# Optimization experiments

Measured on AMD Instinct MI355X. Metric: run time of the kernel, lower is better.

## Reference

```python
import jax, jax.numpy as jnp
import numpy as np

B, P, ENC = 128, 196, 2048
A, E, D, V, L = 512, 512, 512, 10000, 52


def setup_inputs() -> dict:
    key = jax.random.key(0)
    ks = jax.random.split(key, 20)
    encoder_out = jax.random.normal(ks[0], (B, P, ENC), jnp.float32)
    encoded_captions = jax.random.randint(ks[1], (B, L), 0, V)
    lengths = jax.random.randint(ks[2], (B, 1), 20, L + 1)
    lengths = lengths.at[0, 0].set(L)  # guarantee max(decode_lengths) == L-1
    s = 0.05
    return {
        "encoder_out": encoder_out,
        "encoded_captions": encoded_captions,
        "caption_lengths": lengths,
        "emb": jax.random.uniform(ks[3], (V, E), jnp.float32, -0.1, 0.1),
        "We": jax.random.normal(ks[4], (A, ENC)) * s,   # attention.encoder_att
        "be": jnp.zeros((A,), jnp.float32),
        "Wd": jax.random.normal(ks[5], (A, D)) * s,     # attention.decoder_att
        "bd": jnp.zeros((A,), jnp.float32),
        "wf": jax.random.normal(ks[6], (1, A)) * s,     # attention.full_att
        "bf": jnp.zeros((1,), jnp.float32),
        "W_ih": jax.random.normal(ks[7], (4 * D, E + ENC)) * s,
        "b_ih": jnp.zeros((4 * D,), jnp.float32),
        "W_hh": jax.random.normal(ks[8], (4 * D, D)) * s,
        "b_hh": jnp.zeros((4 * D,), jnp.float32),
        "Wbeta": jax.random.normal(ks[9], (ENC, D)) * s,  # f_beta
        "bbeta": jnp.zeros((ENC,), jnp.float32),
        "Wfc": jax.random.uniform(ks[10], (V, D), jnp.float32, -0.1, 0.1),
        "bfc": jnp.zeros((V,), jnp.float32),
    }


def reference(encoder_out, encoded_captions, caption_lengths, emb, We, be, Wd, bd,
              wf, bf, W_ih, b_ih, W_hh, b_hh, Wbeta, bbeta, Wfc, bfc):
    lengths = caption_lengths[:, 0]
    order = jnp.argsort(-lengths)                 # sort descending by length
    lengths = lengths[order]
    enc = encoder_out[order]                      # (B,P,ENC)
    caps = encoded_captions[order]                # (B,L)
    dec_len = lengths - 1                         # decode_lengths
    T = caps.shape[1] - 1                         # max(decode_lengths), static

    embs = emb[caps[:, :T]]                       # (B,T,E)
    embs_t = jnp.transpose(embs, (1, 0, 2))       # (T,B,E)
    active_t = jnp.arange(T)[:, None] < dec_len[None, :]  # (T,B)

    enc_att = jnp.einsum('bpe,ae->bpa', enc, We) + be     # precompute encoder proj
    h0 = jnp.zeros((enc.shape[0], D), enc.dtype)
    c0 = jnp.zeros_like(h0)

    def step(carry, xs):
        h, c = carry
        emb_tok, active = xs                      # (B,E), (B,)
        dec_att = h @ Wd.T + bd                   # (B,A)
        att = jax.nn.relu(enc_att + dec_att[:, None, :])   # (B,P,A)
        scores = jnp.einsum('bpa,a->bp', att, wf[0]) + bf[0]
        alpha = jax.nn.softmax(scores, axis=-1)   # (B,P)
        awe = jnp.einsum('bp,bpe->be', alpha, enc)         # (B,ENC)
        gate = jax.nn.sigmoid(h @ Wbeta.T + bbeta)
        awe = gate * awe
        x = jnp.concatenate([emb_tok, awe], axis=1)        # (B,E+ENC)
        gates = x @ W_ih.T + b_ih + h @ W_hh.T + b_hh      # (B,4D)
        i, f, g, o = jnp.split(gates, 4, axis=1)
        c_new = jax.nn.sigmoid(f) * c + jax.nn.sigmoid(i) * jnp.tanh(g)
        h_new = jax.nn.sigmoid(o) * jnp.tanh(c_new)
        # rows past their decode length keep old state (matches shrinking-batch loop)
        m = active[:, None]
        h = jnp.where(m, h_new, h)
        c = jnp.where(m, c_new, c)
        preds = h_new @ Wfc.T + bfc               # dropout is identity in eval
        preds = jnp.where(m, preds, 0.0)
        return (h, c), preds

    _, preds_t = jax.lax.scan(step, (h0, c0), (embs_t, active_t))
    predictions = jnp.transpose(preds_t, (1, 0, 2))  # (B,T,V)
    return predictions, caps, dec_len
```

## Files before the change

### kernel.cpp

```cpp
#include <hip/hip_runtime.h>
#include <cstdint>
#include <cstddef>

#define B_ 128
#define P_ 196
#define ENC_ 2048
#define A_ 512
#define E_ 512
#define D_ 512
#define V_ 10000
#define L_ 52
#define T_ 51
#define ZPRE 8
#define ZG 8

using short8 = __attribute__((ext_vector_type(8))) short;
using short4v = __attribute__((ext_vector_type(4))) short;
using floatx4 = __attribute__((ext_vector_type(4))) float;

__device__ __forceinline__ float sigf(float x){ return 1.f/(1.f+expf(-x)); }

__device__ __forceinline__ unsigned short f2bf(float f){
  unsigned int u = __float_as_uint(f);
  unsigned int r = (u + 0x7fffu + ((u >> 16) & 1u)) >> 16;
  return (unsigned short)r;
}
__device__ __forceinline__ float bf2f(unsigned short u){
  return __uint_as_float(((unsigned int)u) << 16);
}

__global__ void sort_kernel(const int* __restrict__ cap_len, const int* __restrict__ caps,
                            int* __restrict__ order, int* __restrict__ dec_len,
                            int* __restrict__ caps_sorted,
                            float* __restrict__ out_caps, float* __restrict__ out_declen){
  __shared__ int len_s[B_];
  int i = threadIdx.x;
  len_s[i] = cap_len[i];
  __syncthreads();
  int li = len_s[i];
  int pos = 0;
  for (int j = 0; j < B_; j++){
    int lj = len_s[j];
    pos += (lj > li) || (lj == li && j < i);
  }
  order[pos] = i;
  dec_len[pos] = li - 1;
  out_declen[pos] = (float)(li - 1);
  for (int l = 0; l < L_; l++){
    int v = caps[i * L_ + l];
    caps_sorted[pos * L_ + l] = v;
    out_caps[pos * L_ + l] = (float)v;
  }
}

__global__ void gather_kernel(const float* __restrict__ enc, const int* __restrict__ order,
                              unsigned short* __restrict__ enc_s){
  int b = blockIdx.y;
  int i = (blockIdx.x * 256 + threadIdx.x) * 4;
  const float4 v = *(const float4*)(enc + (size_t)order[b] * (P_ * ENC_) + i);
  short4v r;
  r[0] = (short)f2bf(v.x); r[1] = (short)f2bf(v.y);
  r[2] = (short)f2bf(v.z); r[3] = (short)f2bf(v.w);
  *(short4v*)(enc_s + (size_t)b * (P_ * ENC_) + i) = r;
}

__global__ void prep_kernel(const float* __restrict__ We, const float* __restrict__ Wd,
                            const float* __restrict__ Wbeta,
                            const float* __restrict__ W_ih, const float* __restrict__ W_hh,
                            const float* __restrict__ Wfc,
                            const float* __restrict__ bd, const float* __restrict__ bbeta,
                            const float* __restrict__ b_ih, const float* __restrict__ b_hh,
                            unsigned short* __restrict__ We_b, unsigned short* __restrict__ Wpre_b,
                            unsigned short* __restrict__ Wg_b, unsigned short* __restrict__ Wfc_b,
                            float* __restrict__ bias_pre, float* __restrict__ bias_g,
                            float* __restrict__ h, float* __restrict__ c,
                            unsigned short* __restrict__ h_b, unsigned short* __restrict__ xh){
  unsigned int idx = blockIdx.x * blockDim.x + threadIdx.x;
  unsigned int stride = gridDim.x * blockDim.x;
  for (unsigned int i = idx; i < 512u * 2048u; i += stride) We_b[i] = f2bf(We[i]);
  for (unsigned int i = idx; i < 2560u * 512u; i += stride)
    Wpre_b[i] = f2bf(i < 512u * 512u ? Wd[i] : Wbeta[i - 512u * 512u]);
  for (unsigned int i = idx; i < 2048u * 3072u; i += stride){
    unsigned int j = i / 3072u, k = i - j * 3072u;
    Wg_b[i] = f2bf(k < 2560u ? W_ih[j * 2560u + k] : W_hh[j * 512u + (k - 2560u)]);
  }
  for (unsigned int i = idx; i < 10000u * 512u; i += stride) Wfc_b[i] = f2bf(Wfc[i]);
  for (unsigned int i = idx; i < 2560u; i += stride) bias_pre[i] = (i < 512u) ? bd[i] : bbeta[i - 512u];
  for (unsigned int i = idx; i < 2048u; i += stride) bias_g[i] = b_ih[i] + b_hh[i];
  for (unsigned int i = idx; i < (unsigned)B_ * D_; i += stride){
    h[i] = 0.f; c[i] = 0.f; h_b[i] = 0;
    unsigned int b = i >> 9, d = i & 511u;
    xh[(size_t)b * 3072 + 2560 + d] = 0;
  }
}

#define GEMM_CORE(Aptr, LDA, Bptr, LDB, KDIM, NCLAMP)                         \
  int tid = threadIdx.x; int lane = tid & 63; int w = tid >> 6;               \
  const floatx4 vzero = {0.f,0.f,0.f,0.f};                                    \
  floatx4 acc[4][4];                                                          \
  _Pragma("unroll") for (int i_=0;i_<4;i_++)                                  \
  _Pragma("unroll") for (int j_=0;j_<4;j_++) acc[i_][j_]=vzero;               \
  int mbase=(w&1)<<6, nbase=(w>>1)<<6;                                        \
  int fr=lane&15, fk=(lane>>4)<<3;                                            \
  int rsw_ = (fr&3)<<3;                                                       \
  for (int k0=0;k0<(KDIM);k0+=32){                                            \
    _Pragma("unroll") for (int r_=0;r_<2;r_++){                               \
      int chunk=r_*256+tid; int row=chunk>>2, kc=(chunk&3)<<3;                \
      short8 av=*(const short8*)((Aptr)+(size_t)(m0+row)*(LDA)+k0+kc);        \
      int bn=n0+row; if(bn>(NCLAMP)) bn=(NCLAMP);                             \
      short8 bv=*(const short8*)((Bptr)+(size_t)bn*(LDB)+k0+kc);              \
      int sidx = row*32 + (kc ^ ((row&3)<<3));                                \
      *(short8*)&As[sidx]=av; *(short8*)&Bs[sidx]=bv; }                       \
    __syncthreads();                                                          \
    short8 af[4], bfrag[4];                                                   \
    _Pragma("unroll") for (int i_=0;i_<4;i_++){                               \
      af[i_]=*(const short8*)&As[(mbase+i_*16+fr)*32+(fk^rsw_)];              \
      bfrag[i_]=*(const short8*)&Bs[(nbase+i_*16+fr)*32+(fk^rsw_)]; }         \
    _Pragma("unroll") for (int mi_=0;mi_<4;mi_++)                             \
    _Pragma("unroll") for (int ni_=0;ni_<4;ni_++)                             \
      acc[mi_][ni_]=__builtin_amdgcn_mfma_f32_16x16x32_bf16(af[mi_],bfrag[ni_],acc[mi_][ni_],0,0,0); \
    __syncthreads(); }

__launch_bounds__(256)
__global__ void gemm_bf16(const unsigned short* __restrict__ A, int lda,
                          const unsigned short* __restrict__ Bm, int ldb,
                          const float* __restrict__ bias,
                          float* __restrict__ Cf, unsigned short* __restrict__ Cb, int ldc,
                          int N, int ksz, int epi)
{
  __shared__ unsigned short As[128 * 32];
  __shared__ unsigned short Bs[128 * 32];
  int m0 = blockIdx.y * 128, n0 = blockIdx.x * 128;
  int kb = blockIdx.z * ksz;
  const unsigned short* Ap = A + kb;
  const unsigned short* Bp = Bm + kb;
  GEMM_CORE(Ap, lda, Bp, ldb, ksz, N - 1)
  float* Cz = Cf + (size_t)blockIdx.z * ((size_t)B_ * ldc);
#pragma unroll
  for (int mi = 0; mi < 4; mi++)
#pragma unroll
    for (int ni = 0; ni < 4; ni++){
      floatx4 v = acc[mi][ni];
      int col = n0 + nbase + ni * 16 + fr;
      int rb = m0 + mbase + mi * 16 + ((lane >> 4) << 2);
      if (epi == 0){
#pragma unroll
        for (int r = 0; r < 4; r++)
          Cz[(size_t)(rb + r) * ldc + col] = v[r];
      } else {
        float bb = bias[col];
#pragma unroll
        for (int r = 0; r < 4; r++)
          Cb[(size_t)(rb + r) * ldc + col] = f2bf(v[r] + bb);
      }
    }
}

__launch_bounds__(256)
__global__ void gemm_skinny(const unsigned short* __restrict__ A, int lda,
                            const unsigned short* __restrict__ Bm, int ldb,
                            float* __restrict__ Cf, int ldc, int ksz)
{
  __shared__ unsigned short As[128 * 64];
  __shared__ unsigned short Bs[128 * 64];
  int tid = threadIdx.x; int lane = tid & 63; int w = tid >> 6;
  const floatx4 vzero = {0.f,0.f,0.f,0.f};
  floatx4 acc[4][4];
#pragma unroll
  for (int i_ = 0; i_ < 4; i_++)
#pragma unroll
    for (int j_ = 0; j_ < 4; j_++) acc[i_][j_] = vzero;
  int mbase = (w & 1) << 6, nbase = (w >> 1) << 6;
  int fr = lane & 15, fk = (lane >> 4) << 3;
  int rsw = (fr & 7) << 3;
  int n0 = blockIdx.x * 128;
  int kb = blockIdx.z * ksz;
  const unsigned short* Ap = A + kb;
  const unsigned short* Bp = Bm + kb;
  for (int k0 = 0; k0 < ksz; k0 += 64){
#pragma unroll
    for (int r_ = 0; r_ < 4; r_++){
      int chunk = r_ * 256 + tid;
      int row = chunk >> 3, kc = (chunk & 7) << 3;
      short8 av = *(const short8*)(Ap + (size_t)row * lda + k0 + kc);
      short8 bv = *(const short8*)(Bp + (size_t)(n0 + row) * ldb + k0 + kc);
      int sidx = row * 64 + (kc ^ ((row & 7) << 3));
      *(short8*)&As[sidx] = av;
      *(short8*)&Bs[sidx] = bv;
    }
    __syncthreads();
#pragma unroll
    for (int ks = 0; ks < 2; ks++){
      short8 af[4], bfrag[4];
#pragma unroll
      for (int i_ = 0; i_ < 4; i_++){
        int ra = mbase + i_ * 16 + fr;
        int rb2 = nbase + i_ * 16 + fr;
        af[i_]    = *(const short8*)&As[ra  * 64 + ((ks * 32 + fk) ^ rsw)];
        bfrag[i_] = *(const short8*)&Bs[rb2 * 64 + ((ks * 32 + fk) ^ rsw)];
      }
#pragma unroll
      for (int mi = 0; mi < 4; mi++)
#pragma unroll
        for (int ni = 0; ni < 4; ni++)
          acc[mi][ni] = __builtin_amdgcn_mfma_f32_16x16x32_bf16(af[mi], bfrag[ni], acc[mi][ni], 0, 0, 0);
    }
    __syncthreads();
  }
  float* Cz = Cf + (size_t)blockIdx.z * ((size_t)B_ * ldc);
#pragma unroll
  for (int mi = 0; mi < 4; mi++)
#pragma unroll
    for (int ni = 0; ni < 4; ni++){
      floatx4 v = acc[mi][ni];
      int col = n0 + nbase + ni * 16 + fr;
      int rb = mbase + mi * 16 + ((lane >> 4) << 2);
#pragma unroll
      for (int r = 0; r < 4; r++)
        Cz[(size_t)(rb + r) * ldc + col] = v[r];
    }
}

__launch_bounds__(1024)
__global__ void attn_kernel(const unsigned short* __restrict__ enc_att,
                            const unsigned short* __restrict__ enc_s,
                            const float* __restrict__ ppart,
                            const float* __restrict__ bias_pre,
                            const float* __restrict__ wf, const float* __restrict__ bfp,
                            const float* __restrict__ emb, const int* __restrict__ caps_sorted,
                            unsigned short* __restrict__ xh,
                            int t){
  __shared__ float sc[P_];
  __shared__ float al[P_];
  __shared__ float red[256];
  __shared__ float part2[8][128][8];
  int b = blockIdx.y, bx = blockIdx.x, tid = threadIdx.x;

  int wid = tid >> 6, lane = tid & 63;
  float dav[8], wfv[8];
  {
    const float* bp = bias_pre + lane * 8;
    const float* p0 = ppart + (size_t)b * 2560 + lane * 8;
#pragma unroll
    for (int j = 0; j < 8; j++){
      float s = bp[j];
#pragma unroll
      for (int z = 0; z < ZPRE; z++) s += p0[(size_t)z * (B_ * 2560) + j];
      dav[j] = s;
    }
    *(float4*)&wfv[0] = *(const float4*)(wf + lane * 8);
    *(float4*)&wfv[4] = *(const float4*)(wf + lane * 8 + 4);
  }
  float bfv = bfp[0];
  for (int p = wid; p < P_; p += 16){
    short8 e = *(const short8*)(enc_att + ((size_t)b * P_ + p) * A_ + lane * 8);
    float s = 0.f;
#pragma unroll
    for (int j = 0; j < 8; j++){
      float v = bf2f((unsigned short)e[j]) + dav[j];
      s += fmaxf(v, 0.f) * wfv[j];
    }
#pragma unroll
    for (int off = 32; off > 0; off >>= 1) s += __shfl_down(s, off);
    if (lane == 0) sc[p] = s + bfv;
  }
  __syncthreads();

  if (tid < 256) red[tid] = (tid < P_) ? sc[tid] : -1e30f;
  __syncthreads();
  for (int s = 128; s > 0; s >>= 1){ if (tid < s) red[tid] = fmaxf(red[tid], red[tid + s]); __syncthreads(); }
  float mx = red[0];
  __syncthreads();
  float ex = 0.f;
  if (tid < 256){ ex = (tid < P_) ? expf(sc[tid] - mx) : 0.f; red[tid] = ex; }
  __syncthreads();
  for (int s = 128; s > 0; s >>= 1){ if (tid < s) red[tid] += red[tid + s]; __syncthreads(); }
  float inv = 1.f / red[0];
  if (tid < P_) al[tid] = ex * inv;
  __syncthreads();

  int pg = tid >> 7, et = tid & 127;
  int e0 = bx * 1024 + et * 8;
  const unsigned short* encb = enc_s + (size_t)b * (P_ * ENC_) + e0;
  float aa[8];
#pragma unroll
  for (int j = 0; j < 8; j++) aa[j] = 0.f;
  int pbeg = (pg * 196) >> 3, pend = ((pg + 1) * 196) >> 3;
#pragma unroll 5
  for (int p = pbeg; p < pend; p++){
    float a = al[p];
    short8 v = *(const short8*)(encb + (size_t)p * ENC_);
#pragma unroll
    for (int j = 0; j < 8; j++)
      aa[j] += a * bf2f((unsigned short)v[j]);
  }
#pragma unroll
  for (int j = 0; j < 8; j++) part2[pg][et][j] = aa[j];
  __syncthreads();
  if (pg == 0){
    float s[8];
#pragma unroll
    for (int j = 0; j < 8; j++){
      float acc = 0.f;
#pragma unroll
      for (int g = 0; g < 8; g++) acc += part2[g][et][j];
      s[j] = acc;
    }
    const float* bp = bias_pre + 512 + e0;
    const float* p0 = ppart + (size_t)b * 2560 + 512 + e0;
    short8 r;
#pragma unroll
    for (int j = 0; j < 8; j++){
      float g = bp[j];
#pragma unroll
      for (int z = 0; z < ZPRE; z++) g += p0[(size_t)z * (B_ * 2560) + j];
      r[j] = (short)f2bf(sigf(g) * s[j]);
    }
    *(short8*)(xh + (size_t)b * 3072 + 512 + e0) = r;
  }
  if (bx == 1 && tid < 512){
    int tok = caps_sorted[b * L_ + t];
    xh[(size_t)b * 3072 + tid] = f2bf(emb[(size_t)tok * E_ + tid]);
  }
}

__global__ void lstm_kernel(const float* __restrict__ gpart,
                            const float* __restrict__ bias_g,
                            float* __restrict__ h, float* __restrict__ c,
                            unsigned short* __restrict__ h_b, unsigned short* __restrict__ xh,
                            unsigned short* __restrict__ hnew_b,
                            const int* __restrict__ dec_len, int t){
  int idx = blockIdx.x * 256 + threadIdx.x;
  int b = idx >> 9, d = idx & 511;
  const float* gr = gpart + (size_t)b * 2048;
  float i_ = bias_g[d], f_ = bias_g[512 + d], g_ = bias_g[1024 + d], o_ = bias_g[1536 + d];
#pragma unroll
  for (int z = 0; z < ZG; z++){
    const float* gz = gr + (size_t)z * (B_ * 2048);
    i_ += gz[d]; f_ += gz[512 + d]; g_ += gz[1024 + d]; o_ += gz[1536 + d];
  }
  float cn = sigf(f_) * c[idx] + sigf(i_) * tanhf(g_);
  float hn = sigf(o_) * tanhf(cn);
  bool act = t < dec_len[b];
  float hv = act ? hn : h[idx];
  float cv = act ? cn : c[idx];
  h[idx] = hv; c[idx] = cv;
  unsigned short hvb = f2bf(hv);
  h_b[idx] = hvb;
  xh[(size_t)b * 3072 + 2560 + d] = hvb;
  hnew_b[(size_t)t * (B_ * D_) + idx] = f2bf(hn);
}

__launch_bounds__(256)
__global__ void gemm_preds(const unsigned short* __restrict__ A,
                           const unsigned short* __restrict__ Bm,
                           const float* __restrict__ bias,
                           float* __restrict__ Cf,
                           const int* __restrict__ dec_len){
  __shared__ __attribute__((aligned(16))) char smem[4 * 64 * 68 * 4];
  unsigned short* As = (unsigned short*)smem;
  unsigned short* Bs = (unsigned short*)(smem + 8192);
  int bid = blockIdx.x;
  int xcd = bid & 7, i = bid >> 3;
  int mchunk = xcd >> 1, nchunk = xcd & 1;
  int mi_ = i % 13, ni_ = i / 13;
  int mt = mchunk * 13 + mi_;
  int nt = nchunk * 40 + ni_;
  if (mt >= 51 || nt >= 79) return;
  int m0 = mt * 128, n0 = nt * 128;
  GEMM_CORE(A, D_, Bm, D_, D_, V_ - 1)
  float* Cs = (float*)smem + (size_t)w * (64 * 68);
#pragma unroll
  for (int mi = 0; mi < 4; mi++)
#pragma unroll
    for (int ni = 0; ni < 4; ni++){
      int lc = ni * 16 + fr;
      int col = n0 + nbase + lc;
      float bb = bias[col < V_ ? col : V_ - 1];
#pragma unroll
      for (int r = 0; r < 4; r++){
        int lr = mi * 16 + ((lane >> 4) << 2) + r;
        Cs[lr * 68 + lc] = acc[mi][ni][r] + bb;
      }
    }
#pragma unroll
  for (int rd = 0; rd < 16; rd++){
    int lr = rd * 4 + (lane >> 4);
    int m = m0 + mbase + lr;
    int tt = m >> 7, b = m & 127;
    int col = n0 + nbase + fr * 4;
    floatx4 v = *(const floatx4*)&Cs[lr * 68 + fr * 4];
    if (tt >= dec_len[b]){ v[0] = 0.f; v[1] = 0.f; v[2] = 0.f; v[3] = 0.f; }
    if (col < V_)
      __builtin_nontemporal_store(v, (floatx4*)(Cf + ((size_t)b * T_ + tt) * V_ + col));
  }
}

extern "C" void kernel_launch(void* const* d_in, const int* in_sizes, int n_in,
                              void* d_out, int out_size, void* d_ws, size_t ws_size,
                              hipStream_t stream) {
  const float* encoder_out = (const float*)d_in[0];
  const int*   caps        = (const int*)d_in[1];
  const int*   cap_len     = (const int*)d_in[2];
  const float* emb         = (const float*)d_in[3];
  const float* We          = (const float*)d_in[4];
  const float* be          = (const float*)d_in[5];
  const float* Wd          = (const float*)d_in[6];
  const float* bd          = (const float*)d_in[7];
  const float* wf          = (const float*)d_in[8];
  const float* bf          = (const float*)d_in[9];
  const float* W_ih        = (const float*)d_in[10];
  const float* b_ih        = (const float*)d_in[11];
  const float* W_hh        = (const float*)d_in[12];
  const float* b_hh        = (const float*)d_in[13];
  const float* Wbeta       = (const float*)d_in[14];
  const float* bbeta       = (const float*)d_in[15];
  const float* Wfc         = (const float*)d_in[16];
  const float* bfc         = (const float*)d_in[17];

  float* out_preds  = (float*)d_out;
  float* out_caps   = out_preds + (size_t)B_ * T_ * V_;
  float* out_declen = out_caps + (size_t)B_ * L_;

  char* w = (char*)d_ws;
  auto alloc = [&](size_t bytes) -> void* {
    void* p = (void*)w;
    w += (bytes + 255) & ~(size_t)255;
    return p;
  };
  int*   order       = (int*)alloc(B_ * 4);
  int*   dec_len     = (int*)alloc(B_ * 4);
  int*   caps_sorted = (int*)alloc((size_t)B_ * L_ * 4);
  unsigned short* enc_s   = (unsigned short*)alloc((size_t)B_ * P_ * ENC_ * 2);
  unsigned short* We_b    = (unsigned short*)alloc((size_t)512 * 2048 * 2);
  unsigned short* Wpre_b  = (unsigned short*)alloc((size_t)2560 * 512 * 2);
  unsigned short* Wg_b    = (unsigned short*)alloc((size_t)2048 * 3072 * 2);
  unsigned short* Wfc_b   = (unsigned short*)alloc((size_t)10000 * 512 * 2);
  unsigned short* enc_att = (unsigned short*)alloc((size_t)B_ * P_ * A_ * 2);
  float* bias_pre    = (float*)alloc(2560 * 4);
  float* bias_g      = (float*)alloc(2048 * 4);
  float* ppart       = (float*)alloc((size_t)ZPRE * B_ * 2560 * 4);
  float* gpart       = (float*)alloc((size_t)ZG * B_ * 2048 * 4);
  unsigned short* xh = (unsigned short*)alloc((size_t)B_ * 3072 * 2);
  float* h           = (float*)alloc((size_t)B_ * D_ * 4);
  float* c           = (float*)alloc((size_t)B_ * D_ * 4);
  unsigned short* h_b = (unsigned short*)alloc((size_t)B_ * D_ * 2);
  unsigned short* hnew_b = (unsigned short*)alloc((size_t)T_ * B_ * D_ * 2);

  sort_kernel<<<1, 128, 0, stream>>>(cap_len, caps, order, dec_len, caps_sorted, out_caps, out_declen);
  gather_kernel<<<dim3(392, 128), 256, 0, stream>>>(encoder_out, order, enc_s);
  prep_kernel<<<2048, 256, 0, stream>>>(We, Wd, Wbeta, W_ih, W_hh, Wfc, bd, bbeta, b_ih, b_hh,
                                        We_b, Wpre_b, Wg_b, Wfc_b, bias_pre, bias_g,
                                        h, c, h_b, xh);

  gemm_bf16<<<dim3(4, 196, 1), 256, 0, stream>>>(
      enc_s, ENC_, We_b, ENC_, be, nullptr, enc_att, A_, A_, ENC_, 1);

  for (int t = 0; t < T_; t++){
    gemm_skinny<<<dim3(20, 1, ZPRE), 256, 0, stream>>>(
        h_b, D_, Wpre_b, D_, ppart, 2560, 512 / ZPRE);

    attn_kernel<<<dim3(2, B_), 1024, 0, stream>>>(enc_att, enc_s, ppart, bias_pre, wf, bf,
                                                  emb, caps_sorted, xh, t);

    gemm_skinny<<<dim3(16, 1, ZG), 256, 0, stream>>>(
        xh, 3072, Wg_b, 3072, gpart, 2048, 3072 / ZG);

    lstm_kernel<<<(B_ * D_) / 256, 256, 0, stream>>>(gpart, bias_g, h, c, h_b, xh, hnew_b,
                                                     dec_len, t);
  }

  gemm_preds<<<4160, 256, 0, stream>>>(hnew_b, Wfc_b, bfc, out_preds, dec_len);
}
```

Measured before the change: 3.203 ms.

## Fold W_hh recurrent projection into the pre-attention skinny GEMM

The h·W_hh product moves out of the gate GEMM and into the first per-step skinny GEMM, which now computes h against a stacked [Wd; Wbeta; W_hh] matrix (4608 rows). The gate GEMM's K shrinks from 3072 to 2560, and the LSTM kernel adds the extra split-K partials from ppart. The intent is to shorten the serial gate GEMM on the critical path by doing the h-dependent work in the already-launched earlier GEMM. In exchange, that earlier GEMM grows to 36 column tiles, and the LSTM kernel reads 8 more partial sums per gate. The unused fp32 epilogue path of gemm_bf16 is also removed.

```diff
diff --git a/kernel.cpp b/kernel.cpp
--- a/kernel.cpp
+++ b/kernel.cpp
@@ -13,6 +13,7 @@
 #define T_ 51
 #define ZPRE 8
 #define ZG 8
+#define PLD 4608
 
 using short8 = __attribute__((ext_vector_type(8))) short;
 using short4v = __attribute__((ext_vector_type(4))) short;
@@ -70,27 +71,28 @@
                             const float* __restrict__ Wfc,
                             const float* __restrict__ bd, const float* __restrict__ bbeta,
                             const float* __restrict__ b_ih, const float* __restrict__ b_hh,
-                            unsigned short* __restrict__ We_b, unsigned short* __restrict__ Wpre_b,
+                            unsigned short* __restrict__ We_b, unsigned short* __restrict__ Wpre2_b,
                             unsigned short* __restrict__ Wg_b, unsigned short* __restrict__ Wfc_b,
                             float* __restrict__ bias_pre, float* __restrict__ bias_g,
                             float* __restrict__ h, float* __restrict__ c,
-                            unsigned short* __restrict__ h_b, unsigned short* __restrict__ xh){
+                            unsigned short* __restrict__ h_b){
   unsigned int idx = blockIdx.x * blockDim.x + threadIdx.x;
   unsigned int stride = gridDim.x * blockDim.x;
   for (unsigned int i = idx; i < 512u * 2048u; i += stride) We_b[i] = f2bf(We[i]);
-  for (unsigned int i = idx; i < 2560u * 512u; i += stride)
-    Wpre_b[i] = f2bf(i < 512u * 512u ? Wd[i] : Wbeta[i - 512u * 512u]);
-  for (unsigned int i = idx; i < 2048u * 3072u; i += stride){
-    unsigned int j = i / 3072u, k = i - j * 3072u;
-    Wg_b[i] = f2bf(k < 2560u ? W_ih[j * 2560u + k] : W_hh[j * 512u + (k - 2560u)]);
-  }
+  for (unsigned int i = idx; i < 4608u * 512u; i += stride){
+    unsigned int row = i >> 9, k = i & 511u;
+    float v;
+    if (row < 512u) v = Wd[row * 512u + k];
+    else if (row < 2560u) v = Wbeta[(row - 512u) * 512u + k];
+    else v = W_hh[(size_t)(row - 2560u) * 512u + k];
+    Wpre2_b[i] = f2bf(v);
+  }
+  for (unsigned int i = idx; i < 2048u * 2560u; i += stride) Wg_b[i] = f2bf(W_ih[i]);
   for (unsigned int i = idx; i < 10000u * 512u; i += stride) Wfc_b[i] = f2bf(Wfc[i]);
   for (unsigned int i = idx; i < 2560u; i += stride) bias_pre[i] = (i < 512u) ? bd[i] : bbeta[i - 512u];
   for (unsigned int i = idx; i < 2048u; i += stride) bias_g[i] = b_ih[i] + b_hh[i];
   for (unsigned int i = idx; i < (unsigned)B_ * D_; i += stride){
     h[i] = 0.f; c[i] = 0.f; h_b[i] = 0;
-    unsigned int b = i >> 9, d = i & 511u;
-    xh[(size_t)b * 3072 + 2560 + d] = 0;
   }
 }
 
@@ -125,17 +127,13 @@
 __global__ void gemm_bf16(const unsigned short* __restrict__ A, int lda,
                           const unsigned short* __restrict__ Bm, int ldb,
                           const float* __restrict__ bias,
-                          float* __restrict__ Cf, unsigned short* __restrict__ Cb, int ldc,
-                          int N, int ksz, int epi)
+                          unsigned short* __restrict__ Cb, int ldc,
+                          int N, int ksz)
 {
   __shared__ unsigned short As[128 * 32];
   __shared__ unsigned short Bs[128 * 32];
   int m0 = blockIdx.y * 128, n0 = blockIdx.x * 128;
-  int kb = blockIdx.z * ksz;
-  const unsigned short* Ap = A + kb;
-  const unsigned short* Bp = Bm + kb;
-  GEMM_CORE(Ap, lda, Bp, ldb, ksz, N - 1)
-  float* Cz = Cf + (size_t)blockIdx.z * ((size_t)B_ * ldc);
+  GEMM_CORE(A, lda, Bm, ldb, ksz, N - 1)
 #pragma unroll
   for (int mi = 0; mi < 4; mi++)
 #pragma unroll
@@ -143,16 +141,10 @@
       floatx4 v = acc[mi][ni];
       int col = n0 + nbase + ni * 16 + fr;
       int rb = m0 + mbase + mi * 16 + ((lane >> 4) << 2);
-      if (epi == 0){
-#pragma unroll
-        for (int r = 0; r < 4; r++)
-          Cz[(size_t)(rb + r) * ldc + col] = v[r];
-      } else {
-        float bb = bias[col];
-#pragma unroll
-        for (int r = 0; r < 4; r++)
-          Cb[(size_t)(rb + r) * ldc + col] = f2bf(v[r] + bb);
-      }
+      float bb = bias[col];
+#pragma unroll
+      for (int r = 0; r < 4; r++)
+        Cb[(size_t)(rb + r) * ldc + col] = f2bf(v[r] + bb);
     }
 }
 
@@ -240,12 +232,12 @@
   float dav[8], wfv[8];
   {
     const float* bp = bias_pre + lane * 8;
-    const float* p0 = ppart + (size_t)b * 2560 + lane * 8;
+    const float* p0 = ppart + (size_t)b * PLD + lane * 8;
 #pragma unroll
     for (int j = 0; j < 8; j++){
       float s = bp[j];
 #pragma unroll
-      for (int z = 0; z < ZPRE; z++) s += p0[(size_t)z * (B_ * 2560) + j];
+      for (int z = 0; z < ZPRE; z++) s += p0[(size_t)z * (B_ * PLD) + j];
       dav[j] = s;
     }
     *(float4*)&wfv[0] = *(const float4*)(wf + lane * 8);
@@ -307,37 +299,44 @@
       s[j] = acc;
     }
     const float* bp = bias_pre + 512 + e0;
-    const float* p0 = ppart + (size_t)b * 2560 + 512 + e0;
+    const float* p0 = ppart + (size_t)b * PLD + 512 + e0;
     short8 r;
 #pragma unroll
     for (int j = 0; j < 8; j++){
       float g = bp[j];
 #pragma unroll
-      for (int z = 0; z < ZPRE; z++) g += p0[(size_t)z * (B_ * 2560) + j];
+      for (int z = 0; z < ZPRE; z++) g += p0[(size_t)z * (B_ * PLD) + j];
       r[j] = (short)f2bf(sigf(g) * s[j]);
     }
-    *(short8*)(xh + (size_t)b * 3072 + 512 + e0) = r;
+    *(short8*)(xh + (size_t)b * 2560 + 512 + e0) = r;
   }
   if (bx == 1 && tid < 512){
     int tok = caps_sorted[b * L_ + t];
-    xh[(size_t)b * 3072 + tid] = f2bf(emb[(size_t)tok * E_ + tid]);
+    xh[(size_t)b * 2560 + tid] = f2bf(emb[(size_t)tok * E_ + tid]);
   }
 }
 
 __global__ void lstm_kernel(const float* __restrict__ gpart,
+                            const float* __restrict__ ppart,
                             const float* __restrict__ bias_g,
                             float* __restrict__ h, float* __restrict__ c,
-                            unsigned short* __restrict__ h_b, unsigned short* __restrict__ xh,
+                            unsigned short* __restrict__ h_b,
                             unsigned short* __restrict__ hnew_b,
                             const int* __restrict__ dec_len, int t){
   int idx = blockIdx.x * 256 + threadIdx.x;
   int b = idx >> 9, d = idx & 511;
   const float* gr = gpart + (size_t)b * 2048;
+  const float* pr = ppart + (size_t)b * PLD + 2560;
   float i_ = bias_g[d], f_ = bias_g[512 + d], g_ = bias_g[1024 + d], o_ = bias_g[1536 + d];
 #pragma unroll
   for (int z = 0; z < ZG; z++){
     const float* gz = gr + (size_t)z * (B_ * 2048);
     i_ += gz[d]; f_ += gz[512 + d]; g_ += gz[1024 + d]; o_ += gz[1536 + d];
+  }
+#pragma unroll
+  for (int z = 0; z < ZPRE; z++){
+    const float* pz = pr + (size_t)z * (B_ * PLD);
+    i_ += pz[d]; f_ += pz[512 + d]; g_ += pz[1024 + d]; o_ += pz[1536 + d];
   }
   float cn = sigf(f_) * c[idx] + sigf(i_) * tanhf(g_);
   float hn = sigf(o_) * tanhf(cn);
@@ -345,9 +344,7 @@
   float hv = act ? hn : h[idx];
   float cv = act ? cn : c[idx];
   h[idx] = hv; c[idx] = cv;
-  unsigned short hvb = f2bf(hv);
-  h_b[idx] = hvb;
-  xh[(size_t)b * 3072 + 2560 + d] = hvb;
+  h_b[idx] = f2bf(hv);
   hnew_b[(size_t)t * (B_ * D_) + idx] = f2bf(hn);
 }
 
@@ -433,15 +430,15 @@
   int*   caps_sorted = (int*)alloc((size_t)B_ * L_ * 4);
   unsigned short* enc_s   = (unsigned short*)alloc((size_t)B_ * P_ * ENC_ * 2);
   unsigned short* We_b    = (unsigned short*)alloc((size_t)512 * 2048 * 2);
-  unsigned short* Wpre_b  = (unsigned short*)alloc((size_t)2560 * 512 * 2);
-  unsigned short* Wg_b    = (unsigned short*)alloc((size_t)2048 * 3072 * 2);
+  unsigned short* Wpre2_b = (unsigned short*)alloc((size_t)4608 * 512 * 2);
+  unsigned short* Wg_b    = (unsigned short*)alloc((size_t)2048 * 2560 * 2);
   unsigned short* Wfc_b   = (unsigned short*)alloc((size_t)10000 * 512 * 2);
   unsigned short* enc_att = (unsigned short*)alloc((size_t)B_ * P_ * A_ * 2);
   float* bias_pre    = (float*)alloc(2560 * 4);
   float* bias_g      = (float*)alloc(2048 * 4);
-  float* ppart       = (float*)alloc((size_t)ZPRE * B_ * 2560 * 4);
+  float* ppart       = (float*)alloc((size_t)ZPRE * B_ * PLD * 4);
   float* gpart       = (float*)alloc((size_t)ZG * B_ * 2048 * 4);
-  unsigned short* xh = (unsigned short*)alloc((size_t)B_ * 3072 * 2);
+  unsigned short* xh = (unsigned short*)alloc((size_t)B_ * 2560 * 2);
   float* h           = (float*)alloc((size_t)B_ * D_ * 4);
   float* c           = (float*)alloc((size_t)B_ * D_ * 4);
   unsigned short* h_b = (unsigned short*)alloc((size_t)B_ * D_ * 2);
@@ -450,23 +447,23 @@
   sort_kernel<<<1, 128, 0, stream>>>(cap_len, caps, order, dec_len, caps_sorted, out_caps, out_declen);
   gather_kernel<<<dim3(392, 128), 256, 0, stream>>>(encoder_out, order, enc_s);
   prep_kernel<<<2048, 256, 0, stream>>>(We, Wd, Wbeta, W_ih, W_hh, Wfc, bd, bbeta, b_ih, b_hh,
-                                        We_b, Wpre_b, Wg_b, Wfc_b, bias_pre, bias_g,
-                                        h, c, h_b, xh);
+                                        We_b, Wpre2_b, Wg_b, Wfc_b, bias_pre, bias_g,
+                                        h, c, h_b);
 
   gemm_bf16<<<dim3(4, 196, 1), 256, 0, stream>>>(
-      enc_s, ENC_, We_b, ENC_, be, nullptr, enc_att, A_, A_, ENC_, 1);
+      enc_s, ENC_, We_b, ENC_, be, enc_att, A_, A_, ENC_);
 
   for (int t = 0; t < T_; t++){
-    gemm_skinny<<<dim3(20, 1, ZPRE), 256, 0, stream>>>(
-        h_b, D_, Wpre_b, D_, ppart, 2560, 512 / ZPRE);
+    gemm_skinny<<<dim3(36, 1, ZPRE), 256, 0, stream>>>(
+        h_b, D_, Wpre2_b, D_, ppart, PLD, 512 / ZPRE);
 
     attn_kernel<<<dim3(2, B_), 1024, 0, stream>>>(enc_att, enc_s, ppart, bias_pre, wf, bf,
                                                   emb, caps_sorted, xh, t);
 
     gemm_skinny<<<dim3(16, 1, ZG), 256, 0, stream>>>(
-        xh, 3072, Wg_b, 3072, gpart, 2048, 3072 / ZG);
-
-    lstm_kernel<<<(B_ * D_) / 256, 256, 0, stream>>>(gpart, bias_g, h, c, h_b, xh, hnew_b,
+        xh, 2560, Wg_b, 2560, gpart, 2048, 2560 / ZG);
+
+    lstm_kernel<<<(B_ * D_) / 256, 256, 0, stream>>>(gpart, ppart, bias_g, h, c, h_b, hnew_b,
                                                      dec_len, t);
   }
 
```

Result: slower. 3.622 ms (+13.1%).

## Skip inactive batch rows per timestep and retile skinny GEMMs into 64-row halves

Applied to the files above, without the earlier changes.

Computes the per-timestep count of active sequences, which works because the batch is sorted by length. The skinny recurrent GEMMs are split into two 64-row M halves with a K tile of 128, and a half exits early when none of its rows are active. The attention and LSTM kernels also return early for rows past their decode length, and the pre-attention split-K factor drops from 8 to 4. This cuts wasted compute on finished sequences at late timesteps, at the cost of larger shared memory per GEMM block and a different tile shape.

```diff
diff --git a/kernel.cpp b/kernel.cpp
--- a/kernel.cpp
+++ b/kernel.cpp
@@ -11,7 +11,7 @@
 #define V_ 10000
 #define L_ 52
 #define T_ 51
-#define ZPRE 8
+#define ZPRE 4
 #define ZG 8
 
 using short8 = __attribute__((ext_vector_type(8))) short;
@@ -32,7 +32,8 @@
 __global__ void sort_kernel(const int* __restrict__ cap_len, const int* __restrict__ caps,
                             int* __restrict__ order, int* __restrict__ dec_len,
                             int* __restrict__ caps_sorted,
-                            float* __restrict__ out_caps, float* __restrict__ out_declen){
+                            float* __restrict__ out_caps, float* __restrict__ out_declen,
+                            int* __restrict__ nact){
   __shared__ int len_s[B_];
   int i = threadIdx.x;
   len_s[i] = cap_len[i];
@@ -50,6 +51,11 @@
     int v = caps[i * L_ + l];
     caps_sorted[pos * L_ + l] = v;
     out_caps[pos * L_ + l] = (float)v;
+  }
+  if (i < T_){
+    int cnt = 0;
+    for (int j = 0; j < B_; j++) cnt += (len_s[j] - 1) > i;
+    nact[i] = cnt;
   }
 }
 
@@ -125,17 +131,13 @@
 __global__ void gemm_bf16(const unsigned short* __restrict__ A, int lda,
                           const unsigned short* __restrict__ Bm, int ldb,
                           const float* __restrict__ bias,
-                          float* __restrict__ Cf, unsigned short* __restrict__ Cb, int ldc,
-                          int N, int ksz, int epi)
+                          unsigned short* __restrict__ Cb, int ldc,
+                          int N, int ksz)
 {
   __shared__ unsigned short As[128 * 32];
   __shared__ unsigned short Bs[128 * 32];
   int m0 = blockIdx.y * 128, n0 = blockIdx.x * 128;
-  int kb = blockIdx.z * ksz;
-  const unsigned short* Ap = A + kb;
-  const unsigned short* Bp = Bm + kb;
-  GEMM_CORE(Ap, lda, Bp, ldb, ksz, N - 1)
-  float* Cz = Cf + (size_t)blockIdx.z * ((size_t)B_ * ldc);
+  GEMM_CORE(A, lda, Bm, ldb, ksz, N - 1)
 #pragma unroll
   for (int mi = 0; mi < 4; mi++)
 #pragma unroll
@@ -143,67 +145,67 @@
       floatx4 v = acc[mi][ni];
       int col = n0 + nbase + ni * 16 + fr;
       int rb = m0 + mbase + mi * 16 + ((lane >> 4) << 2);
-      if (epi == 0){
-#pragma unroll
-        for (int r = 0; r < 4; r++)
-          Cz[(size_t)(rb + r) * ldc + col] = v[r];
-      } else {
-        float bb = bias[col];
-#pragma unroll
-        for (int r = 0; r < 4; r++)
-          Cb[(size_t)(rb + r) * ldc + col] = f2bf(v[r] + bb);
-      }
+      float bb = bias[col];
+#pragma unroll
+      for (int r = 0; r < 4; r++)
+        Cb[(size_t)(rb + r) * ldc + col] = f2bf(v[r] + bb);
     }
 }
 
 __launch_bounds__(256)
-__global__ void gemm_skinny(const unsigned short* __restrict__ A, int lda,
-                            const unsigned short* __restrict__ Bm, int ldb,
-                            float* __restrict__ Cf, int ldc, int ksz)
+__global__ void gemm_skinny64(const unsigned short* __restrict__ A, int lda,
+                              const unsigned short* __restrict__ Bm, int ldb,
+                              float* __restrict__ Cf, int ldc, int ksz,
+                              const int* __restrict__ nact, int t)
 {
-  __shared__ unsigned short As[128 * 64];
-  __shared__ unsigned short Bs[128 * 64];
+  __shared__ unsigned short As[64 * 128];
+  __shared__ unsigned short Bs[128 * 128];
+  int my = blockIdx.y;
+  if (my * 64 >= nact[t]) return;
   int tid = threadIdx.x; int lane = tid & 63; int w = tid >> 6;
   const floatx4 vzero = {0.f,0.f,0.f,0.f};
-  floatx4 acc[4][4];
-#pragma unroll
-  for (int i_ = 0; i_ < 4; i_++)
-#pragma unroll
-    for (int j_ = 0; j_ < 4; j_++) acc[i_][j_] = vzero;
-  int mbase = (w & 1) << 6, nbase = (w >> 1) << 6;
+  floatx4 acc[4][2];
+#pragma unroll
+  for (int i_ = 0; i_ < 4; i_++){ acc[i_][0] = vzero; acc[i_][1] = vzero; }
+  int nbase = w << 5;
   int fr = lane & 15, fk = (lane >> 4) << 3;
-  int rsw = (fr & 7) << 3;
+  int rsw = (fr & 15) << 3;
   int n0 = blockIdx.x * 128;
+  int m0g = my * 64;
   int kb = blockIdx.z * ksz;
   const unsigned short* Ap = A + kb;
   const unsigned short* Bp = Bm + kb;
-  for (int k0 = 0; k0 < ksz; k0 += 64){
+  for (int k0 = 0; k0 < ksz; k0 += 128){
 #pragma unroll
     for (int r_ = 0; r_ < 4; r_++){
       int chunk = r_ * 256 + tid;
-      int row = chunk >> 3, kc = (chunk & 7) << 3;
-      short8 av = *(const short8*)(Ap + (size_t)row * lda + k0 + kc);
+      int row = chunk >> 4, kc = (chunk & 15) << 3;
+      short8 av = *(const short8*)(Ap + (size_t)(m0g + row) * lda + k0 + kc);
+      int sidx = row * 128 + (kc ^ ((row & 15) << 3));
+      *(short8*)&As[sidx] = av;
+    }
+#pragma unroll
+    for (int r_ = 0; r_ < 8; r_++){
+      int chunk = r_ * 256 + tid;
+      int row = chunk >> 4, kc = (chunk & 15) << 3;
       short8 bv = *(const short8*)(Bp + (size_t)(n0 + row) * ldb + k0 + kc);
-      int sidx = row * 64 + (kc ^ ((row & 7) << 3));
-      *(short8*)&As[sidx] = av;
+      int sidx = row * 128 + (kc ^ ((row & 15) << 3));
       *(short8*)&Bs[sidx] = bv;
     }
     __syncthreads();
 #pragma unroll
-    for (int ks = 0; ks < 2; ks++){
-      short8 af[4], bfrag[4];
-#pragma unroll
-      for (int i_ = 0; i_ < 4; i_++){
-        int ra = mbase + i_ * 16 + fr;
-        int rb2 = nbase + i_ * 16 + fr;
-        af[i_]    = *(const short8*)&As[ra  * 64 + ((ks * 32 + fk) ^ rsw)];
-        bfrag[i_] = *(const short8*)&Bs[rb2 * 64 + ((ks * 32 + fk) ^ rsw)];
+    for (int ks = 0; ks < 4; ks++){
+      short8 af[4], bfr[2];
+#pragma unroll
+      for (int i_ = 0; i_ < 4; i_++)
+        af[i_] = *(const short8*)&As[(i_ * 16 + fr) * 128 + ((ks * 32 + fk) ^ rsw)];
+      bfr[0] = *(const short8*)&Bs[(nbase + fr) * 128 + ((ks * 32 + fk) ^ rsw)];
+      bfr[1] = *(const short8*)&Bs[(nbase + 16 + fr) * 128 + ((ks * 32 + fk) ^ rsw)];
+#pragma unroll
+      for (int mi = 0; mi < 4; mi++){
+        acc[mi][0] = __builtin_amdgcn_mfma_f32_16x16x32_bf16(af[mi], bfr[0], acc[mi][0], 0, 0, 0);
+        acc[mi][1] = __builtin_amdgcn_mfma_f32_16x16x32_bf16(af[mi], bfr[1], acc[mi][1], 0, 0, 0);
       }
-#pragma unroll
-      for (int mi = 0; mi < 4; mi++)
-#pragma unroll
-        for (int ni = 0; ni < 4; ni++)
-          acc[mi][ni] = __builtin_amdgcn_mfma_f32_16x16x32_bf16(af[mi], bfrag[ni], acc[mi][ni], 0, 0, 0);
     }
     __syncthreads();
   }
@@ -211,10 +213,10 @@
 #pragma unroll
   for (int mi = 0; mi < 4; mi++)
 #pragma unroll
-    for (int ni = 0; ni < 4; ni++){
+    for (int ni = 0; ni < 2; ni++){
       floatx4 v = acc[mi][ni];
       int col = n0 + nbase + ni * 16 + fr;
-      int rb = mbase + mi * 16 + ((lane >> 4) << 2);
+      int rb = m0g + mi * 16 + ((lane >> 4) << 2);
 #pragma unroll
       for (int r = 0; r < 4; r++)
         Cz[(size_t)(rb + r) * ldc + col] = v[r];
@@ -229,12 +231,13 @@
                             const float* __restrict__ wf, const float* __restrict__ bfp,
                             const float* __restrict__ emb, const int* __restrict__ caps_sorted,
                             unsigned short* __restrict__ xh,
-                            int t){
+                            const int* __restrict__ dec_len, int t){
   __shared__ float sc[P_];
   __shared__ float al[P_];
   __shared__ float red[256];
   __shared__ float part2[8][128][8];
   int b = blockIdx.y, bx = blockIdx.x, tid = threadIdx.x;
+  if (t >= dec_len[b]) return;
 
   int wid = tid >> 6, lane = tid & 63;
   float dav[8], wfv[8];
@@ -332,6 +335,7 @@
                             const int* __restrict__ dec_len, int t){
   int idx = blockIdx.x * 256 + threadIdx.x;
   int b = idx >> 9, d = idx & 511;
+  if (t >= dec_len[b]) return;
   const float* gr = gpart + (size_t)b * 2048;
   float i_ = bias_g[d], f_ = bias_g[512 + d], g_ = bias_g[1024 + d], o_ = bias_g[1536 + d];
 #pragma unroll
@@ -341,14 +345,11 @@
   }
   float cn = sigf(f_) * c[idx] + sigf(i_) * tanhf(g_);
   float hn = sigf(o_) * tanhf(cn);
-  bool act = t < dec_len[b];
-  float hv = act ? hn : h[idx];
-  float cv = act ? cn : c[idx];
-  h[idx] = hv; c[idx] = cv;
-  unsigned short hvb = f2bf(hv);
+  h[idx] = hn; c[idx] = cn;
+  unsigned short hvb = f2bf(hn);
   h_b[idx] = hvb;
   xh[(size_t)b * 3072 + 2560 + d] = hvb;
-  hnew_b[(size_t)t * (B_ * D_) + idx] = f2bf(hn);
+  hnew_b[(size_t)t * (B_ * D_) + idx] = hvb;
 }
 
 __launch_bounds__(256)
@@ -430,6 +431,7 @@
   };
   int*   order       = (int*)alloc(B_ * 4);
   int*   dec_len     = (int*)alloc(B_ * 4);
+  int*   nact        = (int*)alloc(64 * 4);
   int*   caps_sorted = (int*)alloc((size_t)B_ * L_ * 4);
   unsigned short* enc_s   = (unsigned short*)alloc((size_t)B_ * P_ * ENC_ * 2);
   unsigned short* We_b    = (unsigned short*)alloc((size_t)512 * 2048 * 2);
@@ -447,24 +449,25 @@
   unsigned short* h_b = (unsigned short*)alloc((size_t)B_ * D_ * 2);
   unsigned short* hnew_b = (unsigned short*)alloc((size_t)T_ * B_ * D_ * 2);
 
-  sort_kernel<<<1, 128, 0, stream>>>(cap_len, caps, order, dec_len, caps_sorted, out_caps, out_declen);
+  sort_kernel<<<1, 128, 0, stream>>>(cap_len, caps, order, dec_len, caps_sorted,
+                                     out_caps, out_declen, nact);
   gather_kernel<<<dim3(392, 128), 256, 0, stream>>>(encoder_out, order, enc_s);
   prep_kernel<<<2048, 256, 0, stream>>>(We, Wd, Wbeta, W_ih, W_hh, Wfc, bd, bbeta, b_ih, b_hh,
                                         We_b, Wpre_b, Wg_b, Wfc_b, bias_pre, bias_g,
                                         h, c, h_b, xh);
 
   gemm_bf16<<<dim3(4, 196, 1), 256, 0, stream>>>(
-      enc_s, ENC_, We_b, ENC_, be, nullptr, enc_att, A_, A_, ENC_, 1);
+      enc_s, ENC_, We_b, ENC_, be, enc_att, A_, A_, ENC_);
 
   for (int t = 0; t < T_; t++){
-    gemm_skinny<<<dim3(20, 1, ZPRE), 256, 0, stream>>>(
-        h_b, D_, Wpre_b, D_, ppart, 2560, 512 / ZPRE);
+    gemm_skinny64<<<dim3(20, 2, ZPRE), 256, 0, stream>>>(
+        h_b, D_, Wpre_b, D_, ppart, 2560, 512 / ZPRE, nact, t);
 
     attn_kernel<<<dim3(2, B_), 1024, 0, stream>>>(enc_att, enc_s, ppart, bias_pre, wf, bf,
-                                                  emb, caps_sorted, xh, t);
-
-    gemm_skinny<<<dim3(16, 1, ZG), 256, 0, stream>>>(
-        xh, 3072, Wg_b, 3072, gpart, 2048, 3072 / ZG);
+                                                  emb, caps_sorted, xh, dec_len, t);
+
+    gemm_skinny64<<<dim3(16, 2, ZG), 256, 0, stream>>>(
+        xh, 3072, Wg_b, 3072, gpart, 2048, 3072 / ZG, nact, t);
 
     lstm_kernel<<<(B_ * D_) / 256, 256, 0, stream>>>(gpart, bias_g, h, c, h_b, xh, hnew_b,
                                                      dec_len, t);
```

Measured after the change: 2.773 ms. 1.16x faster.
